# Optimization experiments

Measured on AMD Instinct MI355X. Metric: run time of the kernel, lower is better.

## Reference

```python
import jax, jax.numpy as jnp
import numpy as np

B, T, D, HD = 4, 4096, 1024, 64

def setup_inputs() -> dict:
    key = jax.random.key(0)
    kx, kq, kk, kv = jax.random.split(key, 4)
    s = 1.0 / np.sqrt(D)
    return {
        "x": jax.random.normal(kx, (B, T, D), dtype=jnp.float32),
        "wq": jax.random.uniform(kq, (HD, D), jnp.float32, -s, s),
        "wk": jax.random.uniform(kk, (HD, D), jnp.float32, -s, s),
        "wv": jax.random.uniform(kv, (HD, D), jnp.float32, -s, s),
    }

def reference(x, wq, wk, wv):
    # Linear(D, headDim, bias=False): y = x @ W.T with W of shape [headDim, D]
    Q = jnp.einsum('btD,dD->btd', x, wq)
    K = jnp.einsum('bsD,dD->bsd', x, wk)
    V = jnp.einsum('bsD,dD->bsd', x, wv)
    head_dim = wq.shape[0]
    logits = jnp.einsum('btd,bsd->bts', Q, K) / jnp.sqrt(jnp.float32(head_dim))
    attn = jax.nn.softmax(logits, axis=-1)
    return jnp.einsum('bts,bsd->btd', attn, V)
```

## Files before the change

kernel.cpp:

```cpp
#include <hip/hip_runtime.h>
#include <math.h>

#define TLEN 4096
#define BD   1024
#define HDIM 64
#define NB   4

typedef __attribute__((ext_vector_type(8))) short bf16x8;
typedef __attribute__((ext_vector_type(4))) float f32x4;

typedef const __attribute__((address_space(1))) unsigned char* gp_t;
typedef __attribute__((address_space(3))) unsigned char* lp_t;

__device__ __forceinline__ void async_cp16(const void* g, void* l) {
    __builtin_amdgcn_global_load_lds((gp_t)g, (lp_t)l, 16, 0, 0);
}

__device__ __forceinline__ unsigned short f2bf(float f) {
    union { float f; unsigned u; } v; v.f = f;
    unsigned r = v.u + 0x7FFF + ((v.u >> 16) & 1);
    return (unsigned short)(r >> 16);
}

__device__ __forceinline__ bf16x8 cvt8(const float4 a, const float4 b) {
    bf16x8 r;
    r[0] = (short)f2bf(a.x); r[1] = (short)f2bf(a.y);
    r[2] = (short)f2bf(a.z); r[3] = (short)f2bf(a.w);
    r[4] = (short)f2bf(b.x); r[5] = (short)f2bf(b.y);
    r[6] = (short)f2bf(b.z); r[7] = (short)f2bf(b.w);
    return r;
}

__global__ __launch_bounds__(256) void wconv_kernel(
    const float* __restrict__ wq, const float* __restrict__ wk,
    const float* __restrict__ wv, unsigned short* __restrict__ wbf)
{
    const int r = blockIdx.x;
    const float* src = (r < 64) ? wq : (r < 128) ? wk : wv;
    const int rr = r & 63;
    const int c  = threadIdx.x * 4;
    float4 a = *(const float4*)&src[(size_t)rr * BD + c];
    uint2 o;
    o.x = (unsigned)f2bf(a.x) | ((unsigned)f2bf(a.y) << 16);
    o.y = (unsigned)f2bf(a.z) | ((unsigned)f2bf(a.w) << 16);
    *(uint2*)&wbf[(size_t)r * BD + c] = o;
}

__global__ __launch_bounds__(256, 1) void qkv_kernel(
    const float* __restrict__ x,
    const unsigned short* __restrict__ wbf,
    unsigned short* __restrict__ Qb,
    unsigned short* __restrict__ Kb,
    unsigned short* __restrict__ Vt)
{
    const int r0   = blockIdx.x * 64;
    const int tid  = threadIdx.x;
    const int lane = tid & 63;
    const int w    = tid >> 6;
    const int g    = lane >> 4;
    const int c    = lane & 15;

    __shared__ __align__(16) unsigned short xb[2][64 * 64];
    __shared__ __align__(16) unsigned short wsh[2][192 * 64];
    __shared__ __align__(16) unsigned short vtr[64][72];

    f32x4 acc[3][4];
    #pragma unroll
    for (int t = 0; t < 3; ++t)
        #pragma unroll
        for (int rg = 0; rg < 4; ++rg) acc[t][rg] = (f32x4){0.f, 0.f, 0.f, 0.f};

    float4 xr[4];

    #define STAGE_W(buf, k0s)                                                   \
        {                                                                       \
            _Pragma("unroll")                                                   \
            for (int ii = 0; ii < 6; ++ii) {                                    \
                const int L   = ii * 256 + tid;                                 \
                const int row = L >> 3;                                         \
                const int jl  = (L & 7) ^ (row & 7);                            \
                async_cp16(&wbf[(size_t)row * BD + (k0s) + jl * 8],             \
                           &wsh[buf][L * 8]);                                   \
            }                                                                   \
        }
    #define LOAD_X(k0s)                                                         \
        {                                                                       \
            _Pragma("unroll")                                                   \
            for (int p = 0; p < 2; ++p) {                                       \
                const int L   = p * 256 + tid;                                  \
                const int row = L >> 3;                                         \
                const int jl  = (L & 7) ^ (row & 7);                            \
                const float* s = &x[(size_t)(r0 + row) * BD + (k0s) + jl * 8];  \
                xr[p * 2]     = *(const float4*)s;                              \
                xr[p * 2 + 1] = *(const float4*)(s + 4);                        \
            }                                                                   \
        }
    #define WRITE_X(buf)                                                        \
        {                                                                       \
            _Pragma("unroll")                                                   \
            for (int p = 0; p < 2; ++p) {                                       \
                const int L = p * 256 + tid;                                    \
                *(bf16x8*)&xb[buf][L * 8] = cvt8(xr[p * 2], xr[p * 2 + 1]);     \
            }                                                                   \
        }

    STAGE_W(0, 0)
    LOAD_X(0)
    WRITE_X(0)

    for (int it = 0; it < 16; ++it) {
        const int cb = it & 1;
        __syncthreads();

        if (it < 15) {
            STAGE_W(cb ^ 1, (it + 1) * 64)
            LOAD_X((it + 1) * 64)
        }

        #pragma unroll
        for (int h = 0; h < 2; ++h) {
            const int slot = ((h * 4 + g) ^ (c & 7)) * 8;
            bf16x8 aX[4], bW[3];
            #pragma unroll
            for (int rg = 0; rg < 4; ++rg)
                aX[rg] = *(const bf16x8*)&xb[cb][(rg * 16 + c) * 64 + slot];
            #pragma unroll
            for (int t = 0; t < 3; ++t)
                bW[t] = *(const bf16x8*)&wsh[cb][((w * 3 + t) * 16 + c) * 64 + slot];
            #pragma unroll
            for (int t = 0; t < 3; ++t)
                #pragma unroll
                for (int rg = 0; rg < 4; ++rg)
                    acc[t][rg] = __builtin_amdgcn_mfma_f32_16x16x32_bf16(
                        aX[rg], bW[t], acc[t][rg], 0, 0, 0);
        }

        if (it < 15) WRITE_X(cb ^ 1)
    }

    const float qscale = 0.18033688f;
    const int   bb     = r0 / TLEN;
    const int   trow   = r0 % TLEN;
    #pragma unroll
    for (int t = 0; t < 3; ++t) {
        const int m = w * 3 + t;
        #pragma unroll
        for (int rg = 0; rg < 4; ++rg)
            #pragma unroll
            for (int i = 0; i < 4; ++i) {
                const int row = rg * 16 + g * 4 + i;
                if (m < 4)
                    Qb[(size_t)(r0 + row) * HDIM + m * 16 + c]
                        = f2bf(acc[t][rg][i] * qscale);
                else if (m < 8)
                    Kb[(size_t)(r0 + row) * HDIM + (m - 4) * 16 + c]
                        = f2bf(acc[t][rg][i]);
                else
                    vtr[(m - 8) * 16 + c][row] = f2bf(acc[t][rg][i]);
            }
    }
    __syncthreads();
    {
        const int d    = tid >> 2;
        const int part = tid & 3;
        uint4 v0 = *(const uint4*)&vtr[d][part * 16];
        uint4 v1 = *(const uint4*)&vtr[d][part * 16 + 8];
        unsigned short* dst = Vt + (size_t)bb * HDIM * TLEN + (size_t)d * TLEN
                            + trow + part * 16;
        *(uint4*)&dst[0] = v0;
        *(uint4*)&dst[8] = v1;
    }
    #undef STAGE_W
    #undef LOAD_X
    #undef WRITE_X
}

template <int KEYS>
__global__ __launch_bounds__(256, 2) void attn_kernel(
    const unsigned short* __restrict__ Qb,
    const unsigned short* __restrict__ Kb,
    const unsigned short* __restrict__ Vt,
    float* __restrict__ O1, float* __restrict__ Ml, float* __restrict__ out)
{
    const int b     = blockIdx.y;
    const int q0    = blockIdx.x * 64;
    const int split = blockIdx.z;
    const int sbase = split * KEYS;

    const unsigned short* Qp = Qb + (size_t)b * TLEN * HDIM;
    const unsigned short* Kp = Kb + (size_t)b * TLEN * HDIM + (size_t)sbase * HDIM;
    const unsigned short* Vp = Vt + (size_t)b * HDIM * TLEN + sbase;

    const int tid  = threadIdx.x;
    const int lane = tid & 63;
    const int w    = tid >> 6;
    const int g    = lane >> 4;
    const int c    = lane & 15;

    __shared__ __align__(16) unsigned short ks[2][4096];
    __shared__ __align__(16) unsigned short vs[2][4096];
    __shared__ __align__(16) unsigned short pp[4][16 * 72];

    bf16x8 qA0 = *(const bf16x8*)&Qp[(size_t)(q0 + w * 16 + c) * HDIM + g * 8];
    bf16x8 qA1 = *(const bf16x8*)&Qp[(size_t)(q0 + w * 16 + c) * HDIM + 32 + g * 8];

    float lsum[4] = {0.f, 0.f, 0.f, 0.f};
    f32x4 oacc[4];
    #pragma unroll
    for (int t = 0; t < 4; ++t) oacc[t] = (f32x4){0.f, 0.f, 0.f, 0.f};

    const int nt = KEYS / 64;

    #pragma unroll
    for (int ii = 0; ii < 2; ++ii) {
        const int L   = ii * 256 + tid;
        const int row = L >> 3;
        const int jl  = (L & 7) ^ (row & 7);
        async_cp16(&Kp[(size_t)row * HDIM + jl * 8], &ks[0][L * 8]);
        async_cp16(&Vp[(size_t)row * TLEN + jl * 8], &vs[0][L * 8]);
    }

    for (int it = 0; it < nt; ++it) {
        const int cb = it & 1;
        __syncthreads();

        if (it + 1 < nt) {
            const int s0  = (it + 1) * 64;
            const int nb2 = cb ^ 1;
            #pragma unroll
            for (int ii = 0; ii < 2; ++ii) {
                const int L   = ii * 256 + tid;
                const int row = L >> 3;
                const int jl  = (L & 7) ^ (row & 7);
                async_cp16(&Kp[(size_t)(s0 + row) * HDIM + jl * 8], &ks[nb2][L * 8]);
                async_cp16(&Vp[(size_t)row * TLEN + s0 + jl * 8],   &vs[nb2][L * 8]);
            }
        }

        f32x4 sacc[4];
        #pragma unroll
        for (int t = 0; t < 4; ++t) sacc[t] = (f32x4){0.f, 0.f, 0.f, 0.f};
        #pragma unroll
        for (int t = 0; t < 4; ++t) {
            const int r  = 16 * t + c;
            const int j0 = g ^ (r & 7);
            bf16x8 kB0 = *(const bf16x8*)&ks[cb][(r * 8 + j0) * 8];
            bf16x8 kB1 = *(const bf16x8*)&ks[cb][(r * 8 + (j0 ^ 4)) * 8];
            sacc[t] = __builtin_amdgcn_mfma_f32_16x16x32_bf16(qA0, kB0, sacc[t], 0, 0, 0);
            sacc[t] = __builtin_amdgcn_mfma_f32_16x16x32_bf16(qA1, kB1, sacc[t], 0, 0, 0);
        }

        #pragma unroll
        for (int i = 0; i < 4; ++i) {
            float p0 = __builtin_amdgcn_exp2f(sacc[0][i]);
            float p1 = __builtin_amdgcn_exp2f(sacc[1][i]);
            float p2 = __builtin_amdgcn_exp2f(sacc[2][i]);
            float p3 = __builtin_amdgcn_exp2f(sacc[3][i]);
            unsigned u0 = __float_as_uint(p0) & 0xffff0000u;
            unsigned u1 = __float_as_uint(p1) & 0xffff0000u;
            unsigned u2 = __float_as_uint(p2) & 0xffff0000u;
            unsigned u3 = __float_as_uint(p3) & 0xffff0000u;
            lsum[i] += (__uint_as_float(u0) + __uint_as_float(u1))
                     + (__uint_as_float(u2) + __uint_as_float(u3));
            unsigned short* pr = &pp[w][(g * 4 + i) * 72 + c];
            pr[0]  = (unsigned short)(u0 >> 16);
            pr[16] = (unsigned short)(u1 >> 16);
            pr[32] = (unsigned short)(u2 >> 16);
            pr[48] = (unsigned short)(u3 >> 16);
        }

        bf16x8 pA0 = *(const bf16x8*)&pp[w][c * 72 + g * 8];
        bf16x8 pA1 = *(const bf16x8*)&pp[w][c * 72 + 32 + g * 8];
        #pragma unroll
        for (int t = 0; t < 4; ++t) {
            const int r  = 16 * t + c;
            const int j0 = g ^ (r & 7);
            bf16x8 vB0 = *(const bf16x8*)&vs[cb][(r * 8 + j0) * 8];
            bf16x8 vB1 = *(const bf16x8*)&vs[cb][(r * 8 + (j0 ^ 4)) * 8];
            oacc[t] = __builtin_amdgcn_mfma_f32_16x16x32_bf16(pA0, vB0, oacc[t], 0, 0, 0);
            oacc[t] = __builtin_amdgcn_mfma_f32_16x16x32_bf16(pA1, vB1, oacc[t], 0, 0, 0);
        }
    }

    #pragma unroll
    for (int i = 0; i < 4; ++i) {
        lsum[i] += __shfl_xor(lsum[i], 1);
        lsum[i] += __shfl_xor(lsum[i], 2);
        lsum[i] += __shfl_xor(lsum[i], 4);
        lsum[i] += __shfl_xor(lsum[i], 8);
    }

    const size_t orow = (size_t)(b * TLEN + q0 + w * 16 + g * 4);
    if (KEYS == TLEN) {
        #pragma unroll
        for (int i = 0; i < 4; ++i) {
            const float inv = 1.0f / lsum[i];
            #pragma unroll
            for (int t = 0; t < 4; ++t)
                out[(orow + i) * HDIM + 16 * t + c] = oacc[t][i] * inv;
        }
    } else {
        float* Od = (split == 0) ? out : O1;
        #pragma unroll
        for (int i = 0; i < 4; ++i)
            #pragma unroll
            for (int t = 0; t < 4; ++t)
                Od[(orow + i) * HDIM + 16 * t + c] = oacc[t][i];
        if (c == 0) {
            #pragma unroll
            for (int i = 0; i < 4; ++i)
                Ml[(size_t)(split * NB + b) * TLEN + q0 + w * 16 + g * 4 + i] = lsum[i];
        }
    }
}

__global__ __launch_bounds__(256) void merge_kernel(
    float* __restrict__ out, const float* __restrict__ O1,
    const float* __restrict__ Ml)
{
    const int idx  = blockIdx.x * 256 + threadIdx.x;
    const int row  = idx >> 4;
    const int col4 = (idx & 15) * 4;
    const int b    = row >> 12;
    const int t    = row & (TLEN - 1);
    const float l0 = Ml[(size_t)b * TLEN + t];
    const float l1 = Ml[(size_t)(NB + b) * TLEN + t];
    const float inv = 1.0f / (l0 + l1);
    float4 a  = *(const float4*)&out[(size_t)row * HDIM + col4];
    float4 bq = *(const float4*)&O1[(size_t)row * HDIM + col4];
    float4 r;
    r.x = (a.x + bq.x) * inv;
    r.y = (a.y + bq.y) * inv;
    r.z = (a.z + bq.z) * inv;
    r.w = (a.w + bq.w) * inv;
    *(float4*)&out[(size_t)row * HDIM + col4] = r;
}

extern "C" void kernel_launch(void* const* d_in, const int* in_sizes, int n_in,
                              void* d_out, int out_size, void* d_ws, size_t ws_size,
                              hipStream_t stream)
{
    (void)in_sizes; (void)n_in; (void)out_size;
    const float* x  = (const float*)d_in[0];
    const float* wq = (const float*)d_in[1];
    const float* wk = (const float*)d_in[2];
    const float* wv = (const float*)d_in[3];
    float* out = (float*)d_out;

    unsigned short* wbf = (unsigned short*)d_out;
    unsigned short* Qbf = (unsigned short*)d_ws;
    unsigned short* Kbf = Qbf + (size_t)NB * TLEN * HDIM;
    unsigned short* Vtb = Kbf + (size_t)NB * TLEN * HDIM;
    float* Ml = (float*)((char*)d_ws + (size_t)3 * NB * TLEN * HDIM * 2);
    float* O1 = Ml + (size_t)2 * NB * TLEN;
    const size_t ws_need_split = (size_t)3 * NB * TLEN * HDIM * 2
                               + (size_t)2 * NB * TLEN * 4
                               + (size_t)NB * TLEN * HDIM * 4;
    const bool use_split = ws_size >= ws_need_split;

    wconv_kernel<<<dim3(192), 256, 0, stream>>>(wq, wk, wv, wbf);
    qkv_kernel<<<dim3(NB * TLEN / 64), 256, 0, stream>>>(x, wbf, Qbf, Kbf, Vtb);

    if (use_split) {
        attn_kernel<TLEN / 2><<<dim3(TLEN / 64, NB, 2), 256, 0, stream>>>(
            Qbf, Kbf, Vtb, O1, Ml, out);
        merge_kernel<<<dim3(NB * TLEN * 16 / 256), 256, 0, stream>>>(out, O1, Ml);
    } else {
        attn_kernel<TLEN><<<dim3(TLEN / 64, NB, 1), 256, 0, stream>>>(
            Qbf, Kbf, Vtb, O1, Ml, out);
    }
}
```

Baseline: 161.1 us.

## Shrink QKV row tile, use 2-wave attention blocks, split keys four ways

The QKV projection kernel now processes 32 rows per block instead of 64, doubling the grid. The attention kernel moves to 128-thread blocks where each wave handles 32 query rows, so each K/V tile loaded to LDS is reused across two 16-row MFMA groups. The key dimension is split four ways instead of two, and the merge kernel sums four partial results. The aim is more blocks and occupancy on the GPU and more reuse per K/V tile, at the cost of extra workspace for partial outputs, more merge traffic and more register pressure per wave.

```diff
diff --git a/kernel.cpp b/kernel.cpp
--- a/kernel.cpp
+++ b/kernel.cpp
@@ -53,24 +53,24 @@
     unsigned short* __restrict__ Kb,
     unsigned short* __restrict__ Vt)
 {
-    const int r0   = blockIdx.x * 64;
+    const int r0   = blockIdx.x * 32;
     const int tid  = threadIdx.x;
     const int lane = tid & 63;
     const int w    = tid >> 6;
     const int g    = lane >> 4;
     const int c    = lane & 15;
 
-    __shared__ __align__(16) unsigned short xb[2][64 * 64];
+    __shared__ __align__(16) unsigned short xb[2][32 * 64];
     __shared__ __align__(16) unsigned short wsh[2][192 * 64];
-    __shared__ __align__(16) unsigned short vtr[64][72];
-
-    f32x4 acc[3][4];
+    __shared__ __align__(16) unsigned short vtr[64][40];
+
+    f32x4 acc[3][2];
     #pragma unroll
     for (int t = 0; t < 3; ++t)
         #pragma unroll
-        for (int rg = 0; rg < 4; ++rg) acc[t][rg] = (f32x4){0.f, 0.f, 0.f, 0.f};
-
-    float4 xr[4];
+        for (int rg = 0; rg < 2; ++rg) acc[t][rg] = (f32x4){0.f, 0.f, 0.f, 0.f};
+
+    float4 xr0, xr1;
 
     #define STAGE_W(buf, k0s)                                                   \
         {                                                                       \
@@ -85,24 +85,14 @@
         }
     #define LOAD_X(k0s)                                                         \
         {                                                                       \
-            _Pragma("unroll")                                                   \
-            for (int p = 0; p < 2; ++p) {                                       \
-                const int L   = p * 256 + tid;                                  \
-                const int row = L >> 3;                                         \
-                const int jl  = (L & 7) ^ (row & 7);                            \
-                const float* s = &x[(size_t)(r0 + row) * BD + (k0s) + jl * 8];  \
-                xr[p * 2]     = *(const float4*)s;                              \
-                xr[p * 2 + 1] = *(const float4*)(s + 4);                        \
-            }                                                                   \
+            const int row = tid >> 3;                                           \
+            const int jl  = (tid & 7) ^ (row & 7);                              \
+            const float* s = &x[(size_t)(r0 + row) * BD + (k0s) + jl * 8];      \
+            xr0 = *(const float4*)s;                                            \
+            xr1 = *(const float4*)(s + 4);                                      \
         }
     #define WRITE_X(buf)                                                        \
-        {                                                                       \
-            _Pragma("unroll")                                                   \
-            for (int p = 0; p < 2; ++p) {                                       \
-                const int L = p * 256 + tid;                                    \
-                *(bf16x8*)&xb[buf][L * 8] = cvt8(xr[p * 2], xr[p * 2 + 1]);     \
-            }                                                                   \
-        }
+        { *(bf16x8*)&xb[buf][tid * 8] = cvt8(xr0, xr1); }
 
     STAGE_W(0, 0)
     LOAD_X(0)
@@ -120,9 +110,9 @@
         #pragma unroll
         for (int h = 0; h < 2; ++h) {
             const int slot = ((h * 4 + g) ^ (c & 7)) * 8;
-            bf16x8 aX[4], bW[3];
-            #pragma unroll
-            for (int rg = 0; rg < 4; ++rg)
+            bf16x8 aX[2], bW[3];
+            #pragma unroll
+            for (int rg = 0; rg < 2; ++rg)
                 aX[rg] = *(const bf16x8*)&xb[cb][(rg * 16 + c) * 64 + slot];
             #pragma unroll
             for (int t = 0; t < 3; ++t)
@@ -130,7 +120,7 @@
             #pragma unroll
             for (int t = 0; t < 3; ++t)
                 #pragma unroll
-                for (int rg = 0; rg < 4; ++rg)
+                for (int rg = 0; rg < 2; ++rg)
                     acc[t][rg] = __builtin_amdgcn_mfma_f32_16x16x32_bf16(
                         aX[rg], bW[t], acc[t][rg], 0, 0, 0);
         }
@@ -145,7 +135,7 @@
     for (int t = 0; t < 3; ++t) {
         const int m = w * 3 + t;
         #pragma unroll
-        for (int rg = 0; rg < 4; ++rg)
+        for (int rg = 0; rg < 2; ++rg)
             #pragma unroll
             for (int i = 0; i < 4; ++i) {
                 const int row = rg * 16 + g * 4 + i;
@@ -163,12 +153,10 @@
     {
         const int d    = tid >> 2;
         const int part = tid & 3;
-        uint4 v0 = *(const uint4*)&vtr[d][part * 16];
-        uint4 v1 = *(const uint4*)&vtr[d][part * 16 + 8];
+        uint4 v0 = *(const uint4*)&vtr[d][part * 8];
         unsigned short* dst = Vt + (size_t)bb * HDIM * TLEN + (size_t)d * TLEN
-                            + trow + part * 16;
+                            + trow + part * 8;
         *(uint4*)&dst[0] = v0;
-        *(uint4*)&dst[8] = v1;
     }
     #undef STAGE_W
     #undef LOAD_X
@@ -176,7 +164,7 @@
 }
 
 template <int KEYS>
-__global__ __launch_bounds__(256, 2) void attn_kernel(
+__global__ __launch_bounds__(128, 1) void attn_kernel(
     const unsigned short* __restrict__ Qb,
     const unsigned short* __restrict__ Kb,
     const unsigned short* __restrict__ Vt,
@@ -199,21 +187,28 @@
 
     __shared__ __align__(16) unsigned short ks[2][4096];
     __shared__ __align__(16) unsigned short vs[2][4096];
-    __shared__ __align__(16) unsigned short pp[4][16 * 72];
-
-    bf16x8 qA0 = *(const bf16x8*)&Qp[(size_t)(q0 + w * 16 + c) * HDIM + g * 8];
-    bf16x8 qA1 = *(const bf16x8*)&Qp[(size_t)(q0 + w * 16 + c) * HDIM + 32 + g * 8];
-
-    float lsum[4] = {0.f, 0.f, 0.f, 0.f};
-    f32x4 oacc[4];
-    #pragma unroll
-    for (int t = 0; t < 4; ++t) oacc[t] = (f32x4){0.f, 0.f, 0.f, 0.f};
+    __shared__ __align__(16) unsigned short pp[64][72];
+
+    bf16x8 qA[2][2];
+    #pragma unroll
+    for (int h = 0; h < 2; ++h)
+        #pragma unroll
+        for (int kk = 0; kk < 2; ++kk)
+            qA[h][kk] = *(const bf16x8*)
+                &Qp[(size_t)(q0 + w * 32 + h * 16 + c) * HDIM + kk * 32 + g * 8];
+
+    float lsum[2][4] = {};
+    f32x4 oacc[2][4];
+    #pragma unroll
+    for (int h = 0; h < 2; ++h)
+        #pragma unroll
+        for (int t = 0; t < 4; ++t) oacc[h][t] = (f32x4){0.f, 0.f, 0.f, 0.f};
 
     const int nt = KEYS / 64;
 
     #pragma unroll
-    for (int ii = 0; ii < 2; ++ii) {
-        const int L   = ii * 256 + tid;
+    for (int ii = 0; ii < 4; ++ii) {
+        const int L   = ii * 128 + tid;
         const int row = L >> 3;
         const int jl  = (L & 7) ^ (row & 7);
         async_cp16(&Kp[(size_t)row * HDIM + jl * 8], &ks[0][L * 8]);
@@ -228,8 +223,8 @@
             const int s0  = (it + 1) * 64;
             const int nb2 = cb ^ 1;
             #pragma unroll
-            for (int ii = 0; ii < 2; ++ii) {
-                const int L   = ii * 256 + tid;
+            for (int ii = 0; ii < 4; ++ii) {
+                const int L   = ii * 128 + tid;
                 const int row = L >> 3;
                 const int jl  = (L & 7) ^ (row & 7);
                 async_cp16(&Kp[(size_t)(s0 + row) * HDIM + jl * 8], &ks[nb2][L * 8]);
@@ -237,79 +232,104 @@
             }
         }
 
-        f32x4 sacc[4];
-        #pragma unroll
-        for (int t = 0; t < 4; ++t) sacc[t] = (f32x4){0.f, 0.f, 0.f, 0.f};
+        f32x4 sacc[2][4];
+        #pragma unroll
+        for (int h = 0; h < 2; ++h)
+            #pragma unroll
+            for (int t = 0; t < 4; ++t) sacc[h][t] = (f32x4){0.f, 0.f, 0.f, 0.f};
         #pragma unroll
         for (int t = 0; t < 4; ++t) {
             const int r  = 16 * t + c;
             const int j0 = g ^ (r & 7);
             bf16x8 kB0 = *(const bf16x8*)&ks[cb][(r * 8 + j0) * 8];
             bf16x8 kB1 = *(const bf16x8*)&ks[cb][(r * 8 + (j0 ^ 4)) * 8];
-            sacc[t] = __builtin_amdgcn_mfma_f32_16x16x32_bf16(qA0, kB0, sacc[t], 0, 0, 0);
-            sacc[t] = __builtin_amdgcn_mfma_f32_16x16x32_bf16(qA1, kB1, sacc[t], 0, 0, 0);
-        }
-
-        #pragma unroll
-        for (int i = 0; i < 4; ++i) {
-            float p0 = __builtin_amdgcn_exp2f(sacc[0][i]);
-            float p1 = __builtin_amdgcn_exp2f(sacc[1][i]);
-            float p2 = __builtin_amdgcn_exp2f(sacc[2][i]);
-            float p3 = __builtin_amdgcn_exp2f(sacc[3][i]);
-            unsigned u0 = __float_as_uint(p0) & 0xffff0000u;
-            unsigned u1 = __float_as_uint(p1) & 0xffff0000u;
-            unsigned u2 = __float_as_uint(p2) & 0xffff0000u;
-            unsigned u3 = __float_as_uint(p3) & 0xffff0000u;
-            lsum[i] += (__uint_as_float(u0) + __uint_as_float(u1))
-                     + (__uint_as_float(u2) + __uint_as_float(u3));
-            unsigned short* pr = &pp[w][(g * 4 + i) * 72 + c];
-            pr[0]  = (unsigned short)(u0 >> 16);
-            pr[16] = (unsigned short)(u1 >> 16);
-            pr[32] = (unsigned short)(u2 >> 16);
-            pr[48] = (unsigned short)(u3 >> 16);
-        }
-
-        bf16x8 pA0 = *(const bf16x8*)&pp[w][c * 72 + g * 8];
-        bf16x8 pA1 = *(const bf16x8*)&pp[w][c * 72 + 32 + g * 8];
+            #pragma unroll
+            for (int h = 0; h < 2; ++h) {
+                sacc[h][t] = __builtin_amdgcn_mfma_f32_16x16x32_bf16(
+                    qA[h][0], kB0, sacc[h][t], 0, 0, 0);
+                sacc[h][t] = __builtin_amdgcn_mfma_f32_16x16x32_bf16(
+                    qA[h][1], kB1, sacc[h][t], 0, 0, 0);
+            }
+        }
+
+        #pragma unroll
+        for (int h = 0; h < 2; ++h)
+            #pragma unroll
+            for (int i = 0; i < 4; ++i) {
+                float p0 = __builtin_amdgcn_exp2f(sacc[h][0][i]);
+                float p1 = __builtin_amdgcn_exp2f(sacc[h][1][i]);
+                float p2 = __builtin_amdgcn_exp2f(sacc[h][2][i]);
+                float p3 = __builtin_amdgcn_exp2f(sacc[h][3][i]);
+                unsigned u0 = __float_as_uint(p0) & 0xffff0000u;
+                unsigned u1 = __float_as_uint(p1) & 0xffff0000u;
+                unsigned u2 = __float_as_uint(p2) & 0xffff0000u;
+                unsigned u3 = __float_as_uint(p3) & 0xffff0000u;
+                lsum[h][i] += (__uint_as_float(u0) + __uint_as_float(u1))
+                            + (__uint_as_float(u2) + __uint_as_float(u3));
+                unsigned short* pr = &pp[w * 32 + h * 16 + g * 4 + i][c];
+                pr[0]  = (unsigned short)(u0 >> 16);
+                pr[16] = (unsigned short)(u1 >> 16);
+                pr[32] = (unsigned short)(u2 >> 16);
+                pr[48] = (unsigned short)(u3 >> 16);
+            }
+
+        bf16x8 pA[2][2];
+        #pragma unroll
+        for (int h = 0; h < 2; ++h) {
+            pA[h][0] = *(const bf16x8*)&pp[w * 32 + h * 16 + c][g * 8];
+            pA[h][1] = *(const bf16x8*)&pp[w * 32 + h * 16 + c][32 + g * 8];
+        }
         #pragma unroll
         for (int t = 0; t < 4; ++t) {
             const int r  = 16 * t + c;
             const int j0 = g ^ (r & 7);
             bf16x8 vB0 = *(const bf16x8*)&vs[cb][(r * 8 + j0) * 8];
             bf16x8 vB1 = *(const bf16x8*)&vs[cb][(r * 8 + (j0 ^ 4)) * 8];
-            oacc[t] = __builtin_amdgcn_mfma_f32_16x16x32_bf16(pA0, vB0, oacc[t], 0, 0, 0);
-            oacc[t] = __builtin_amdgcn_mfma_f32_16x16x32_bf16(pA1, vB1, oacc[t], 0, 0, 0);
-        }
-    }
-
-    #pragma unroll
-    for (int i = 0; i < 4; ++i) {
-        lsum[i] += __shfl_xor(lsum[i], 1);
-        lsum[i] += __shfl_xor(lsum[i], 2);
-        lsum[i] += __shfl_xor(lsum[i], 4);
-        lsum[i] += __shfl_xor(lsum[i], 8);
-    }
-
-    const size_t orow = (size_t)(b * TLEN + q0 + w * 16 + g * 4);
-    if (KEYS == TLEN) {
+            #pragma unroll
+            for (int h = 0; h < 2; ++h) {
+                oacc[h][t] = __builtin_amdgcn_mfma_f32_16x16x32_bf16(
+                    pA[h][0], vB0, oacc[h][t], 0, 0, 0);
+                oacc[h][t] = __builtin_amdgcn_mfma_f32_16x16x32_bf16(
+                    pA[h][1], vB1, oacc[h][t], 0, 0, 0);
+            }
+        }
+    }
+
+    #pragma unroll
+    for (int h = 0; h < 2; ++h)
         #pragma unroll
         for (int i = 0; i < 4; ++i) {
-            const float inv = 1.0f / lsum[i];
-            #pragma unroll
-            for (int t = 0; t < 4; ++t)
-                out[(orow + i) * HDIM + 16 * t + c] = oacc[t][i] * inv;
-        }
-    } else {
-        float* Od = (split == 0) ? out : O1;
-        #pragma unroll
-        for (int i = 0; i < 4; ++i)
-            #pragma unroll
-            for (int t = 0; t < 4; ++t)
-                Od[(orow + i) * HDIM + 16 * t + c] = oacc[t][i];
-        if (c == 0) {
+            lsum[h][i] += __shfl_xor(lsum[h][i], 1);
+            lsum[h][i] += __shfl_xor(lsum[h][i], 2);
+            lsum[h][i] += __shfl_xor(lsum[h][i], 4);
+            lsum[h][i] += __shfl_xor(lsum[h][i], 8);
+        }
+
+    #pragma unroll
+    for (int h = 0; h < 2; ++h) {
+        const size_t orow = (size_t)(b * TLEN + q0 + w * 32 + h * 16 + g * 4);
+        if (KEYS == TLEN) {
+            #pragma unroll
+            for (int i = 0; i < 4; ++i) {
+                const float inv = 1.0f / lsum[h][i];
+                #pragma unroll
+                for (int t = 0; t < 4; ++t)
+                    out[(orow + i) * HDIM + 16 * t + c] = oacc[h][t][i] * inv;
+            }
+        } else {
+            float* Od = (split == 0)
+                ? out : O1 + (size_t)(split - 1) * NB * TLEN * HDIM;
             #pragma unroll
             for (int i = 0; i < 4; ++i)
-                Ml[(size_t)(split * NB + b) * TLEN + q0 + w * 16 + g * 4 + i] = lsum[i];
+                #pragma unroll
+                for (int t = 0; t < 4; ++t)
+                    Od[(orow + i) * HDIM + 16 * t + c] = oacc[h][t][i];
+            if (c == 0) {
+                #pragma unroll
+                for (int i = 0; i < 4; ++i)
+                    Ml[(size_t)(split * NB + b) * TLEN
+                       + q0 + w * 32 + h * 16 + g * 4 + i] = lsum[h][i];
+            }
         }
     }
 }
@@ -323,17 +343,19 @@
     const int col4 = (idx & 15) * 4;
     const int b    = row >> 12;
     const int t    = row & (TLEN - 1);
-    const float l0 = Ml[(size_t)b * TLEN + t];
-    const float l1 = Ml[(size_t)(NB + b) * TLEN + t];
-    const float inv = 1.0f / (l0 + l1);
-    float4 a  = *(const float4*)&out[(size_t)row * HDIM + col4];
-    float4 bq = *(const float4*)&O1[(size_t)row * HDIM + col4];
-    float4 r;
-    r.x = (a.x + bq.x) * inv;
-    r.y = (a.y + bq.y) * inv;
-    r.z = (a.z + bq.z) * inv;
-    r.w = (a.w + bq.w) * inv;
-    *(float4*)&out[(size_t)row * HDIM + col4] = r;
+    float l = 0.f;
+    #pragma unroll
+    for (int s = 0; s < 4; ++s) l += Ml[(size_t)(s * NB + b) * TLEN + t];
+    const float inv = 1.0f / l;
+    float4 a = *(const float4*)&out[(size_t)row * HDIM + col4];
+    #pragma unroll
+    for (int s = 1; s < 4; ++s) {
+        float4 p = *(const float4*)
+            &O1[(size_t)(s - 1) * NB * TLEN * HDIM + (size_t)row * HDIM + col4];
+        a.x += p.x; a.y += p.y; a.z += p.z; a.w += p.w;
+    }
+    a.x *= inv; a.y *= inv; a.z *= inv; a.w *= inv;
+    *(float4*)&out[(size_t)row * HDIM + col4] = a;
 }
 
 extern "C" void kernel_launch(void* const* d_in, const int* in_sizes, int n_in,
@@ -352,21 +374,21 @@
     unsigned short* Kbf = Qbf + (size_t)NB * TLEN * HDIM;
     unsigned short* Vtb = Kbf + (size_t)NB * TLEN * HDIM;
     float* Ml = (float*)((char*)d_ws + (size_t)3 * NB * TLEN * HDIM * 2);
-    float* O1 = Ml + (size_t)2 * NB * TLEN;
-    const size_t ws_need_split = (size_t)3 * NB * TLEN * HDIM * 2
-                               + (size_t)2 * NB * TLEN * 4
-                               + (size_t)NB * TLEN * HDIM * 4;
-    const bool use_split = ws_size >= ws_need_split;
+    float* O1 = Ml + (size_t)4 * NB * TLEN;
+    const size_t ws_need = (size_t)3 * NB * TLEN * HDIM * 2
+                         + (size_t)4 * NB * TLEN * 4
+                         + (size_t)3 * NB * TLEN * HDIM * 4;
+    const bool use_split = ws_size >= ws_need;
 
     wconv_kernel<<<dim3(192), 256, 0, stream>>>(wq, wk, wv, wbf);
-    qkv_kernel<<<dim3(NB * TLEN / 64), 256, 0, stream>>>(x, wbf, Qbf, Kbf, Vtb);
+    qkv_kernel<<<dim3(NB * TLEN / 32), 256, 0, stream>>>(x, wbf, Qbf, Kbf, Vtb);
 
     if (use_split) {
-        attn_kernel<TLEN / 2><<<dim3(TLEN / 64, NB, 2), 256, 0, stream>>>(
+        attn_kernel<TLEN / 4><<<dim3(TLEN / 64, NB, 4), 128, 0, stream>>>(
             Qbf, Kbf, Vtb, O1, Ml, out);
         merge_kernel<<<dim3(NB * TLEN * 16 / 256), 256, 0, stream>>>(out, O1, Ml);
     } else {
-        attn_kernel<TLEN><<<dim3(TLEN / 64, NB, 1), 256, 0, stream>>>(
+        attn_kernel<TLEN><<<dim3(TLEN / 64, NB, 1), 128, 0, stream>>>(
             Qbf, Kbf, Vtb, O1, Ml, out);
     }
 }
```

Result: slower. 171.6 us (+6.5%).
